# Performance work log

Measured on AMD Instinct MI355X. Metric: run time of the kernel, lower is better.

The kernel has to match this reference:

```python
import jax, jax.numpy as jnp
import numpy as np

B, M, H = 8, 2048, 1024


def setup_inputs() -> dict:
    key = jax.random.key(0)
    k0, k1, k2, k3, k4 = jax.random.split(key, 5)
    return {
        "query": jax.random.normal(k0, (B, M, H), dtype=jnp.float32),
        "key": jax.random.normal(k1, (B, M, H), dtype=jnp.float32),
        "span": jax.random.uniform(k2, (B, M, 2), dtype=jnp.float32),
        "value": jax.random.normal(k3, (B, M, H), dtype=jnp.float32),
        "key_pe": jax.random.normal(k4, (1, H, M), dtype=jnp.float32),
    }


def reference(query, key, span, value, key_pe):
    # Faithful to the source's returned value:
    #   attn_cont (span-gathered version) is overwritten by the dense q @ k^T,
    #   and the scaled/softmaxed `attn` (content + positional) is computed but
    #   NEVER used for the output. The module returns attn_cont @ value with
    #   no scaling and no softmax. span / key_pe do not affect the output.
    attn_cont = jnp.einsum('bmh,bnh->bmn', query, key)  # [B, M, M]
    out = jnp.matmul(attn_cont, value)                   # [B, M, H]
    return out
```

## Files before the change

kernel.cpp:

```cpp
#include <hip/hip_runtime.h>
#include <hip/hip_bf16.h>

typedef __attribute__((ext_vector_type(4))) float f32x4;
typedef __attribute__((ext_vector_type(8))) short bf16x8;
typedef __attribute__((ext_vector_type(2))) unsigned int u32x2;
typedef unsigned short u16;
typedef unsigned int u32;


__device__ __forceinline__ u16 f2bf(float f) {
  union { float f; unsigned int u; } v;
  v.f = f;
  unsigned int r = (v.u + 0x7fffu + ((v.u >> 16) & 1u)) >> 16;
  return (u16)r;
}

__device__ __forceinline__ u32 pk2(float a, float b) {
  u32 r;
  asm("v_cvt_pk_bf16_f32 %0, %1, %2" : "=v"(r) : "v"(a), "v"(b));
  return r;
}

__device__ __forceinline__ void async16(const void* g, const void* l) {
  __builtin_amdgcn_global_load_lds(
      (const __attribute__((address_space(1))) unsigned int*)(unsigned long)g,
      (__attribute__((address_space(3))) unsigned int*)(unsigned int)(unsigned long)l,
      16, 0, 0);
}

__device__ __forceinline__ void bar() {
  asm volatile("" ::: "memory");
  __builtin_amdgcn_s_barrier();
  asm volatile("" ::: "memory");
}

#define WAIT_VM0() asm volatile("s_waitcnt vmcnt(0)" ::: "memory")

__global__ __launch_bounds__(256) void cvt_all(const float* __restrict__ Kin,
                                               const float* __restrict__ Vin,
                                               const float* __restrict__ Q,
                                               u16* __restrict__ Kt,
                                               u16* __restrict__ Vt,
                                               u16* __restrict__ Qb) {
  __shared__ char tile[16384];
  const int z = blockIdx.y;
  const int t = threadIdx.x;

  if (z < 16) {
    const int bsel = z >> 1;
    const float* in = (z & 1) ? Kin : Vin;
    u16* out = (z & 1) ? Kt : Vt;
    const long bo = (long)bsel * 2048 * 1024;
    const int s = blockIdx.x;
    const float* src = in + bo + (long)s * 8 * 1024;

    f32x4 v[8];
#pragma unroll
    for (int i = 0; i < 8; ++i)
      v[i] = *(const f32x4*)(src + i * 1024 + t * 4);

#pragma unroll
    for (int q = 0; q < 4; ++q) {
      const int c = t * 4 + q;
      const int val = c ^ ((c >> 3) & 7);
      union { u32 w[4]; uint4 u4; } U;
      U.w[0] = pk2(v[0][q], v[1][q]);
      U.w[1] = pk2(v[2][q], v[3][q]);
      U.w[2] = pk2(v[4][q], v[5][q]);
      U.w[3] = pk2(v[6][q], v[7][q]);
      *(uint4*)(tile + ((long)val << 4)) = U.u4;
    }
    __syncthreads();

    u16* dst = out + bo + (long)s * 8192;
#pragma unroll
    for (int p = 0; p < 4; ++p) {
      const int u = t + p * 256;
      const int val = u ^ ((u >> 3) & 7);
      uint4 r = *(const uint4*)(tile + ((long)val << 4));
      *(uint4*)(dst + (long)u * 8) = r;
    }
  } else {
    const int qb = z - 16;
    const float* src = Q + (long)qb * 2048 * 1024 + (long)blockIdx.x * 8192;
    u16* dst = Qb + (long)qb * 2048 * 1024 + (long)blockIdx.x * 8192;
#pragma unroll
    for (int i = 0; i < 8; ++i) {
      f32x4 v = *(const f32x4*)(src + (t + i * 256) * 4);
      u32x2 w; w.x = pk2(v.x, v.y); w.y = pk2(v.z, v.w);
      *(u32x2*)(dst + (long)(t + i * 256) * 4) = w;
    }
  }
}

__global__ __launch_bounds__(512, 2) void gemmA(const u16* __restrict__ Vt,
                                                const u16* __restrict__ Kt,
                                                u16* __restrict__ Pt) {
  __shared__ u16 As[2][8][256][8];
  __shared__ u16 Bs[2][8][128][8];

  const int bid = blockIdx.x;
  const int b = bid & 7;
  const int tile = bid >> 3;
  const int bn0 = (tile & 7) * 128;
  const int bm0 = (tile >> 3) * 256;

  const int tid = threadIdx.x;
  const int lane = tid & 63;
  const int wave = tid >> 6;
  const int wr = wave >> 2;
  const int wc = wave & 3;
  const int l16 = lane & 15;
  const int kh = lane >> 4;

  const char* Ab = (const char*)(Vt + (long)b * 1024 * 2048);
  const char* Bb = (const char*)(Kt + (long)b * 1024 * 2048);

  int aoff[4], boff[2];
#pragma unroll
  for (int i = 0; i < 4; ++i) {
    int u = tid + i * 512;
    aoff[i] = (u >> 8) * 16384 + (bm0 + (u & 255)) * 16;
  }
#pragma unroll
  for (int i = 0; i < 2; ++i) {
    int u = tid + i * 512;
    boff[i] = (u >> 7) * 16384 + (bn0 + (u & 127)) * 16;
  }

#define STG_A(buf)                                                             \
  {                                                                            \
    _Pragma("unroll") for (int i_ = 0; i_ < 4; ++i_) {                         \
      async16(Ab + aoff[i_], (char*)&As[buf][0][0][0] + (tid + i_ * 512) * 16);\
      aoff[i_] += 131072;                                                      \
    }                                                                          \
  }
#define STG_B(buf)                                                             \
  {                                                                            \
    _Pragma("unroll") for (int i_ = 0; i_ < 2; ++i_) {                         \
      async16(Bb + boff[i_], (char*)&Bs[buf][0][0][0] + (tid + i_ * 512) * 16);\
      boff[i_] += 131072;                                                      \
    }                                                                          \
  }

  int offA[2][4][2];
#pragma unroll
  for (int q = 0; q < 2; ++q)
#pragma unroll
    for (int f = 0; f < 4; ++f)
#pragma unroll
      for (int ks = 0; ks < 2; ++ks)
        offA[q][f][ks] =
            (ks * 4 + kh) * 4096 + (q * 128 + wr * 64 + f * 16 + l16) * 16;
  int offB[2][2];
#pragma unroll
  for (int fn = 0; fn < 2; ++fn)
#pragma unroll
    for (int ks = 0; ks < 2; ++ks)
      offB[fn][ks] = (ks * 4 + kh) * 2048 + (fn * 64 + wc * 16 + l16) * 16;

  f32x4 acc[8][2] = {};
  bf16x8 ar[4][2], br[2][2];

  STG_A(0); STG_B(0);
  WAIT_VM0();
  bar();

  const int NT = 32;
  for (int t = 0; t < NT; ++t) {
    const int cur = t & 1, nxt = cur ^ 1;
    const bool g = (t + 1 < NT);
    const char* Abuf = (const char*)&As[cur][0][0][0];
    const char* Bbuf = (const char*)&Bs[cur][0][0][0];

#pragma unroll
    for (int f = 0; f < 4; ++f)
#pragma unroll
      for (int ks = 0; ks < 2; ++ks)
        ar[f][ks] = *(const bf16x8*)(Abuf + offA[0][f][ks]);
#pragma unroll
    for (int fn = 0; fn < 2; ++fn)
#pragma unroll
      for (int ks = 0; ks < 2; ++ks)
        br[fn][ks] = *(const bf16x8*)(Bbuf + offB[fn][ks]);

    if (g) { STG_A(nxt); STG_B(nxt); }

    __builtin_amdgcn_s_setprio(1);
#pragma unroll
    for (int f = 0; f < 4; ++f)
#pragma unroll
      for (int n = 0; n < 2; ++n)
#pragma unroll
        for (int ks = 0; ks < 2; ++ks)
          acc[f][n] = __builtin_amdgcn_mfma_f32_16x16x32_bf16(
              ar[f][ks], br[n][ks], acc[f][n], 0, 0, 0);
    __builtin_amdgcn_s_setprio(0);

#pragma unroll
    for (int f = 0; f < 4; ++f)
#pragma unroll
      for (int ks = 0; ks < 2; ++ks)
        ar[f][ks] = *(const bf16x8*)(Abuf + offA[1][f][ks]);

    __builtin_amdgcn_s_setprio(1);
#pragma unroll
    for (int f = 0; f < 4; ++f)
#pragma unroll
      for (int n = 0; n < 2; ++n)
#pragma unroll
        for (int ks = 0; ks < 2; ++ks)
          acc[4 + f][n] = __builtin_amdgcn_mfma_f32_16x16x32_bf16(
              ar[f][ks], br[n][ks], acc[4 + f][n], 0, 0, 0);
    __builtin_amdgcn_s_setprio(0);

    if (g) WAIT_VM0();
    bar();
  }
#undef STG_A
#undef STG_B

  u16* Cb = Pt + (long)b * 1024 * 1024;
#pragma unroll
  for (int fm = 0; fm < 8; ++fm) {
    const int gm = bm0 + (fm >> 2) * 128 + wr * 64 + (fm & 3) * 16 + kh * 4;
#pragma unroll
    for (int fn = 0; fn < 2; ++fn) {
#pragma unroll
      for (int r = 0; r < 4; ++r)
        Cb[(long)((bn0 >> 6) + fn) * 65536 + (long)(gm + r) * 64 +
           wc * 16 + l16] = f2bf(acc[fm][fn][r]);
    }
  }
}

__global__ __launch_bounds__(512, 2) void gemmB(const u16* __restrict__ A,
                                                const u16* __restrict__ Bt,
                                                float* __restrict__ out) {
  __shared__ u16 As[2][256][64];
  __shared__ u16 Bs[2][128][64];

  const int bid = blockIdx.x;
  const int b = bid & 7;
  const int tile = bid >> 3;
  const int bn0 = (tile & 7) * 128;
  const int bm0 = (tile >> 3) * 256;

  const int tid = threadIdx.x;
  const int lane = tid & 63;
  const int wave = tid >> 6;
  const int wr = wave >> 2;
  const int wc = wave & 3;
  const int l16 = lane & 15;
  const int kh = lane >> 4;

  const char* Ab = (const char*)(A + (long)b * 2048 * 1024);
  const char* Bb = (const char*)(Bt + (long)b * 1024 * 1024);

  int aoff[4], boff[2];
#pragma unroll
  for (int i = 0; i < 4; ++i) {
    int u = tid + i * 512;
    int row = u >> 3, sl = (u & 7) ^ (row & 7);
    aoff[i] = (bm0 + row) * 2048 + sl * 16;
  }
#pragma unroll
  for (int i = 0; i < 2; ++i) {
    int u = tid + i * 512;
    int row = u >> 3, sl = (u & 7) ^ (row & 7);
    boff[i] = (bn0 + row) * 128 + sl * 16;
  }

#define STG_A(buf)                                                          \
  {                                                                         \
    _Pragma("unroll") for (int i_ = 0; i_ < 4; ++i_) {                      \
      async16(Ab + aoff[i_], (char*)&As[buf][0][0] + (tid + i_ * 512) * 16);\
      aoff[i_] += 128;                                                      \
    }                                                                       \
  }
#define STG_B(buf)                                                          \
  {                                                                         \
    _Pragma("unroll") for (int i_ = 0; i_ < 2; ++i_) {                      \
      async16(Bb + boff[i_], (char*)&Bs[buf][0][0] + (tid + i_ * 512) * 16);\
      boff[i_] += 131072;                                                   \
    }                                                                       \
  }

  int offA[2][4][2];
#pragma unroll
  for (int q = 0; q < 2; ++q)
#pragma unroll
    for (int f = 0; f < 4; ++f) {
      int r = q * 128 + wr * 64 + f * 16 + l16;
#pragma unroll
      for (int ks = 0; ks < 2; ++ks)
        offA[q][f][ks] = r * 64 + (((ks * 4 + kh) ^ (l16 & 7)) * 8);
    }
  int offB[2][2];
#pragma unroll
  for (int fn = 0; fn < 2; ++fn) {
    int r = fn * 64 + wc * 16 + l16;
#pragma unroll
    for (int ks = 0; ks < 2; ++ks)
      offB[fn][ks] = r * 64 + (((ks * 4 + kh) ^ (l16 & 7)) * 8);
  }

  f32x4 acc[8][2] = {};
  bf16x8 ar[4][2], br[2][2];

  STG_A(0); STG_B(0);
  WAIT_VM0();
  bar();

  const int NT = 16;
  for (int t = 0; t < NT; ++t) {
    const int cur = t & 1, nxt = cur ^ 1;
    const bool g = (t + 1 < NT);
    const u16* Abuf = &As[cur][0][0];
    const u16* Bbuf = &Bs[cur][0][0];

#pragma unroll
    for (int f = 0; f < 4; ++f)
#pragma unroll
      for (int ks = 0; ks < 2; ++ks)
        ar[f][ks] = *(const bf16x8*)(Abuf + offA[0][f][ks]);
#pragma unroll
    for (int fn = 0; fn < 2; ++fn)
#pragma unroll
      for (int ks = 0; ks < 2; ++ks)
        br[fn][ks] = *(const bf16x8*)(Bbuf + offB[fn][ks]);

    if (g) { STG_A(nxt); STG_B(nxt); }

    __builtin_amdgcn_s_setprio(1);
#pragma unroll
    for (int f = 0; f < 4; ++f)
#pragma unroll
      for (int n = 0; n < 2; ++n)
#pragma unroll
        for (int ks = 0; ks < 2; ++ks)
          acc[f][n] = __builtin_amdgcn_mfma_f32_16x16x32_bf16(
              ar[f][ks], br[n][ks], acc[f][n], 0, 0, 0);
    __builtin_amdgcn_s_setprio(0);

#pragma unroll
    for (int f = 0; f < 4; ++f)
#pragma unroll
      for (int ks = 0; ks < 2; ++ks)
        ar[f][ks] = *(const bf16x8*)(Abuf + offA[1][f][ks]);

    __builtin_amdgcn_s_setprio(1);
#pragma unroll
    for (int f = 0; f < 4; ++f)
#pragma unroll
      for (int n = 0; n < 2; ++n)
#pragma unroll
        for (int ks = 0; ks < 2; ++ks)
          acc[4 + f][n] = __builtin_amdgcn_mfma_f32_16x16x32_bf16(
              ar[f][ks], br[n][ks], acc[4 + f][n], 0, 0, 0);
    __builtin_amdgcn_s_setprio(0);

    if (g) WAIT_VM0();
    bar();
  }
#undef STG_A
#undef STG_B

  float* Cf = out + (long)b * 2048 * 1024;
#pragma unroll
  for (int fm = 0; fm < 8; ++fm) {
    const int gm = bm0 + (fm >> 2) * 128 + wr * 64 + (fm & 3) * 16 + kh * 4;
#pragma unroll
    for (int fn = 0; fn < 2; ++fn) {
      const int gn = bn0 + fn * 64 + wc * 16 + l16;
#pragma unroll
      for (int r = 0; r < 4; ++r)
        Cf[(long)(gm + r) * 1024 + gn] = acc[fm][fn][r];
    }
  }
}


extern "C" void kernel_launch(void* const* d_in, const int* in_sizes, int n_in,
                              void* d_out, int out_size, void* d_ws, size_t ws_size,
                              hipStream_t stream) {
  const float* Q  = (const float*)d_in[0];
  const float* Kf = (const float*)d_in[1];
  const float* V  = (const float*)d_in[3];
  float* out = (float*)d_out;

  char* ws = (char*)d_ws;
  u16* Vt = (u16*)(ws);
  u16* Kt = (u16*)(ws + (size_t)32 * 1024 * 1024);
  u16* Pt = (u16*)(ws + (size_t)64 * 1024 * 1024);
  u16* Qb = (u16*)(ws + (size_t)80 * 1024 * 1024);

  cvt_all<<<dim3(256, 24), 256, 0, stream>>>(Kf, V, Q, Kt, Vt, Qb);

  gemmA<<<256, 512, 0, stream>>>(Vt, Kt, Pt);

  gemmB<<<512, 512, 0, stream>>>(Qb, Pt, out);
}
```

Before: 130.8 us.

## Fuse Q fp32-to-bf16 conversion into gemmB's A-tile load path

Removes the separate Q conversion pass from the conversion kernel. gemmB now loads fp32 Q from global memory into registers, packs it to bf16, and writes it into swizzled LDS, interleaved with the MFMA phases. This avoids writing and re-reading a bf16 copy of Q (about 32MB of traffic). In exchange gemmB reads twice the A bytes per tile, uses more registers, and adds an LDS write plus lgkmcnt wait in the main loop, which could hurt latency hiding.

```diff
diff --git a/kernel.cpp b/kernel.cpp
--- a/kernel.cpp
+++ b/kernel.cpp
@@ -34,62 +34,49 @@
   asm volatile("" ::: "memory");
 }
 
-#define WAIT_VM0() asm volatile("s_waitcnt vmcnt(0)" ::: "memory")
-
-__global__ __launch_bounds__(256) void cvt_all(const float* __restrict__ Kin,
-                                               const float* __restrict__ Vin,
-                                               const float* __restrict__ Q,
-                                               u16* __restrict__ Kt,
-                                               u16* __restrict__ Vt,
-                                               u16* __restrict__ Qb) {
+#define WAIT_VM0()   asm volatile("s_waitcnt vmcnt(0)" ::: "memory")
+#define WAIT_LGKM0() asm volatile("s_waitcnt lgkmcnt(0)" ::: "memory")
+
+__global__ __launch_bounds__(256) void cvt_kv(const float* __restrict__ Kin,
+                                              const float* __restrict__ Vin,
+                                              u16* __restrict__ Kt,
+                                              u16* __restrict__ Vt) {
   __shared__ char tile[16384];
   const int z = blockIdx.y;
   const int t = threadIdx.x;
 
-  if (z < 16) {
-    const int bsel = z >> 1;
-    const float* in = (z & 1) ? Kin : Vin;
-    u16* out = (z & 1) ? Kt : Vt;
-    const long bo = (long)bsel * 2048 * 1024;
-    const int s = blockIdx.x;
-    const float* src = in + bo + (long)s * 8 * 1024;
-
-    f32x4 v[8];
-#pragma unroll
-    for (int i = 0; i < 8; ++i)
-      v[i] = *(const f32x4*)(src + i * 1024 + t * 4);
-
-#pragma unroll
-    for (int q = 0; q < 4; ++q) {
-      const int c = t * 4 + q;
-      const int val = c ^ ((c >> 3) & 7);
-      union { u32 w[4]; uint4 u4; } U;
-      U.w[0] = pk2(v[0][q], v[1][q]);
-      U.w[1] = pk2(v[2][q], v[3][q]);
-      U.w[2] = pk2(v[4][q], v[5][q]);
-      U.w[3] = pk2(v[6][q], v[7][q]);
-      *(uint4*)(tile + ((long)val << 4)) = U.u4;
-    }
-    __syncthreads();
-
-    u16* dst = out + bo + (long)s * 8192;
-#pragma unroll
-    for (int p = 0; p < 4; ++p) {
-      const int u = t + p * 256;
-      const int val = u ^ ((u >> 3) & 7);
-      uint4 r = *(const uint4*)(tile + ((long)val << 4));
-      *(uint4*)(dst + (long)u * 8) = r;
-    }
-  } else {
-    const int qb = z - 16;
-    const float* src = Q + (long)qb * 2048 * 1024 + (long)blockIdx.x * 8192;
-    u16* dst = Qb + (long)qb * 2048 * 1024 + (long)blockIdx.x * 8192;
-#pragma unroll
-    for (int i = 0; i < 8; ++i) {
-      f32x4 v = *(const f32x4*)(src + (t + i * 256) * 4);
-      u32x2 w; w.x = pk2(v.x, v.y); w.y = pk2(v.z, v.w);
-      *(u32x2*)(dst + (long)(t + i * 256) * 4) = w;
-    }
+  const int bsel = z >> 1;
+  const float* in = (z & 1) ? Kin : Vin;
+  u16* out = (z & 1) ? Kt : Vt;
+  const long bo = (long)bsel * 2048 * 1024;
+  const int s = blockIdx.x;
+  const float* src = in + bo + (long)s * 8 * 1024;
+
+  f32x4 v[8];
+#pragma unroll
+  for (int i = 0; i < 8; ++i)
+    v[i] = *(const f32x4*)(src + i * 1024 + t * 4);
+
+#pragma unroll
+  for (int q = 0; q < 4; ++q) {
+    const int c = t * 4 + q;
+    const int val = c ^ ((c >> 3) & 7);
+    union { u32 w[4]; uint4 u4; } U;
+    U.w[0] = pk2(v[0][q], v[1][q]);
+    U.w[1] = pk2(v[2][q], v[3][q]);
+    U.w[2] = pk2(v[4][q], v[5][q]);
+    U.w[3] = pk2(v[6][q], v[7][q]);
+    *(uint4*)(tile + ((long)val << 4)) = U.u4;
+  }
+  __syncthreads();
+
+  u16* dst = out + bo + (long)s * 8192;
+#pragma unroll
+  for (int p = 0; p < 4; ++p) {
+    const int u = t + p * 256;
+    const int val = u ^ ((u >> 3) & 7);
+    uint4 r = *(const uint4*)(tile + ((long)val << 4));
+    *(uint4*)(dst + (long)u * 8) = r;
   }
 }
 
@@ -234,7 +221,7 @@
   }
 }
 
-__global__ __launch_bounds__(512, 2) void gemmB(const u16* __restrict__ A,
+__global__ __launch_bounds__(512, 2) void gemmB(const float* __restrict__ Qf,
                                                 const u16* __restrict__ Bt,
                                                 float* __restrict__ out) {
   __shared__ u16 As[2][256][64];
@@ -254,16 +241,19 @@
   const int l16 = lane & 15;
   const int kh = lane >> 4;
 
-  const char* Ab = (const char*)(A + (long)b * 2048 * 1024);
   const char* Bb = (const char*)(Bt + (long)b * 1024 * 1024);
 
-  int aoff[4], boff[2];
+  const float* qsrc[4];
+  int awo[4];
 #pragma unroll
   for (int i = 0; i < 4; ++i) {
-    int u = tid + i * 512;
-    int row = u >> 3, sl = (u & 7) ^ (row & 7);
-    aoff[i] = (bm0 + row) * 2048 + sl * 16;
-  }
+    int U = tid + i * 512;
+    int r = U >> 3, s = U & 7;
+    qsrc[i] = Qf + (long)b * 2048 * 1024 + (long)(bm0 + r) * 1024 + s * 8;
+    awo[i] = (r * 64 + (s ^ (r & 7)) * 8) * 2;
+  }
+
+  int boff[2];
 #pragma unroll
   for (int i = 0; i < 2; ++i) {
     int u = tid + i * 512;
@@ -271,11 +261,24 @@
     boff[i] = (bn0 + row) * 128 + sl * 16;
   }
 
-#define STG_A(buf)                                                          \
+#define LOAD_Q()                                                            \
   {                                                                         \
     _Pragma("unroll") for (int i_ = 0; i_ < 4; ++i_) {                      \
-      async16(Ab + aoff[i_], (char*)&As[buf][0][0] + (tid + i_ * 512) * 16);\
-      aoff[i_] += 128;                                                      \
+      qlo[i_] = *(const f32x4*)(qsrc[i_]);                                  \
+      qhi[i_] = *(const f32x4*)(qsrc[i_] + 4);                              \
+      qsrc[i_] += 64;                                                       \
+    }                                                                       \
+  }
+#define WRITE_Q(buf)                                                        \
+  {                                                                         \
+    char* dA_ = (char*)&As[buf][0][0];                                      \
+    _Pragma("unroll") for (int i_ = 0; i_ < 4; ++i_) {                      \
+      union { u32 w[4]; uint4 u4; } U_;                                     \
+      U_.w[0] = pk2(qlo[i_].x, qlo[i_].y);                                  \
+      U_.w[1] = pk2(qlo[i_].z, qlo[i_].w);                                  \
+      U_.w[2] = pk2(qhi[i_].x, qhi[i_].y);                                  \
+      U_.w[3] = pk2(qhi[i_].z, qhi[i_].w);                                  \
+      *(uint4*)(dA_ + awo[i_]) = U_.u4;                                     \
     }                                                                       \
   }
 #define STG_B(buf)                                                          \
@@ -306,10 +309,14 @@
   }
 
   f32x4 acc[8][2] = {};
+  f32x4 qlo[4], qhi[4];
   bf16x8 ar[4][2], br[2][2];
 
-  STG_A(0); STG_B(0);
+  LOAD_Q();
+  STG_B(0);
+  WRITE_Q(0);
   WAIT_VM0();
+  WAIT_LGKM0();
   bar();
 
   const int NT = 16;
@@ -330,7 +337,10 @@
       for (int ks = 0; ks < 2; ++ks)
         br[fn][ks] = *(const bf16x8*)(Bbuf + offB[fn][ks]);
 
-    if (g) { STG_A(nxt); STG_B(nxt); }
+    if (g) {
+      LOAD_Q();
+      STG_B(nxt);
+    }
 
     __builtin_amdgcn_s_setprio(1);
 #pragma unroll
@@ -349,6 +359,8 @@
       for (int ks = 0; ks < 2; ++ks)
         ar[f][ks] = *(const bf16x8*)(Abuf + offA[1][f][ks]);
 
+    if (g) WRITE_Q(nxt);
+
     __builtin_amdgcn_s_setprio(1);
 #pragma unroll
     for (int f = 0; f < 4; ++f)
@@ -361,9 +373,11 @@
     __builtin_amdgcn_s_setprio(0);
 
     if (g) WAIT_VM0();
+    WAIT_LGKM0();
     bar();
   }
-#undef STG_A
+#undef LOAD_Q
+#undef WRITE_Q
 #undef STG_B
 
   float* Cf = out + (long)b * 2048 * 1024;
@@ -393,11 +407,10 @@
   u16* Vt = (u16*)(ws);
   u16* Kt = (u16*)(ws + (size_t)32 * 1024 * 1024);
   u16* Pt = (u16*)(ws + (size_t)64 * 1024 * 1024);
-  u16* Qb = (u16*)(ws + (size_t)80 * 1024 * 1024);
-
-  cvt_all<<<dim3(256, 24), 256, 0, stream>>>(Kf, V, Q, Kt, Vt, Qb);
+
+  cvt_kv<<<dim3(256, 16), 256, 0, stream>>>(Kf, V, Kt, Vt);
 
   gemmA<<<256, 512, 0, stream>>>(Vt, Kt, Pt);
 
-  gemmB<<<512, 512, 0, stream>>>(Qb, Pt, out);
-}
+  gemmB<<<512, 512, 0, stream>>>(Q, Pt, out);
+}
```

Result: slower. 148.3 us (+13.4%).
